# Performance work log

Measured on AMD Instinct MI355X. Metric: run time of the kernel, lower is better.

## Reference

```python
import jax, jax.numpy as jnp
import numpy as np

NUM_HEADS = 16
NUM_FEATURES = 1024
HEAD_DIM = NUM_FEATURES // NUM_HEADS
B, S = 2, 2048


def setup_inputs() -> dict:
    key = jax.random.key(0)
    ks = jax.random.split(key, 12)
    d = NUM_FEATURES
    scale = 1.0 / np.sqrt(d)
    inp = {
        'q': jax.random.normal(ks[0], (B, S, d), jnp.float32),
        'v': jax.random.normal(ks[1], (B, S, d), jnp.float32),
        'k': jax.random.normal(ks[2], (B, S, d), jnp.float32),
        'mask': jnp.ones((1, 1, S, S), jnp.float32),
        # Dense params: flax kernel layout (in, out)
        'Wq': jax.random.normal(ks[3], (d, d), jnp.float32) * scale,
        'bq': jnp.zeros((d,), jnp.float32),
        'Wv': jax.random.normal(ks[4], (d, d), jnp.float32) * scale,
        'bv': jnp.zeros((d,), jnp.float32),
        'Wk': jax.random.normal(ks[5], (d, d), jnp.float32) * scale,
        'bk': jnp.zeros((d,), jnp.float32),
        'Wo': jax.random.normal(ks[6], (d, d), jnp.float32) * scale,
        'bo': jnp.zeros((d,), jnp.float32),
    }
    return inp


def _split_heads(x):
    b, s, _ = x.shape
    return jnp.transpose(x.reshape(b, s, NUM_HEADS, HEAD_DIM), (0, 2, 1, 3))  # [B,H,S,Dh]


def reference(q, v, k, mask, Wq, bq, Wv, bv, Wk, bk, Wo, bo):
    q = q @ Wq + bq
    v = v @ Wv + bv
    k = k @ Wk + bk
    qh = _split_heads(q) / jnp.sqrt(jnp.float32(NUM_FEATURES))  # note: sqrt(d_model), as in source
    kh = _split_heads(k)
    vh = _split_heads(v)
    logits = jnp.einsum('bhqd,bhkd->bhqk', qh, kh)
    logits = logits - 1e9 * (1.0 - mask)
    weights = jax.nn.softmax(logits, axis=-1)
    # dropout deterministic (eval_mode=True) -> identity
    out = jnp.einsum('bhqk,bhkd->bhqd', weights, vh)
    out = jnp.transpose(out, (0, 2, 1, 3)).reshape(q.shape[0], q.shape[1], NUM_FEATURES)
    return out @ Wo + bo
```

## Files before the change

### kernel.cpp

```cpp
#include <hip/hip_runtime.h>
#include <hip/hip_bf16.h>


namespace {
constexpr int DM = 1024;
constexpr int NH = 16;
constexpr int HD = 64;
constexpr int SQ = 2048;
constexpr int M_TOT = 2 * SQ;

using f32x4  = __attribute__((ext_vector_type(4))) float;
using f32x16 = __attribute__((ext_vector_type(16))) float;
using bf16x8 = __attribute__((ext_vector_type(8))) short;
using u16 = unsigned short;

__device__ __forceinline__ u16 f2bf(float f) {
  union { float f; unsigned u; } x; x.f = f;
  unsigned r = x.u + 0x7fffu + ((x.u >> 16) & 1u);
  return (u16)(r >> 16);
}

__device__ __forceinline__ unsigned pk2(float lo, float hi) {
  unsigned r;
  asm("v_cvt_pk_bf16_f32 %0, %1, %2" : "=v"(r) : "v"(lo), "v"(hi));
  return r;
}

__device__ __forceinline__ float fexp2(float x) {
  float r;
  asm("v_exp_f32 %0, %1" : "=v"(r) : "v"(x));
  return r;
}

__device__ __forceinline__ float m3(float a, float b, float c) {
  float r;
  asm("v_max3_f32 %0, %1, %2, %3" : "=v"(r) : "v"(a), "v"(b), "v"(c));
  return r;
}

__device__ __forceinline__ f32x16 mfma32(bf16x8 a, bf16x8 b, f32x16 c) {
  return __builtin_amdgcn_mfma_f32_32x32x16_bf16(a, b, c, 0, 0, 0);
}

__device__ __forceinline__ void gld16(const void* g, void* l) {
  __builtin_amdgcn_global_load_lds((const __attribute__((address_space(1))) void*)g,
                                   (__attribute__((address_space(3))) void*)l, 16, 0, 0);
}
}

__global__ __launch_bounds__(256) void tobf_kernel(const float* __restrict__ q,
                                                   const float* __restrict__ k,
                                                   const float* __restrict__ v,
                                                   u16* __restrict__ out) {
  const float* src = blockIdx.y == 0 ? q : (blockIdx.y == 1 ? k : v);
  u16* dst = out + (size_t)blockIdx.y * M_TOT * DM;
  size_t i = ((size_t)blockIdx.x * 256 + threadIdx.x) * 8;
  float4 a = *(const float4*)(src + i), b = *(const float4*)(src + i + 4);
  union { u16 us[8]; uint4 v4; } pk;
  pk.us[0] = f2bf(a.x); pk.us[1] = f2bf(a.y); pk.us[2] = f2bf(a.z); pk.us[3] = f2bf(a.w);
  pk.us[4] = f2bf(b.x); pk.us[5] = f2bf(b.y); pk.us[6] = f2bf(b.z); pk.us[7] = f2bf(b.w);
  *(uint4*)(dst + i) = pk.v4;
}

__global__ __launch_bounds__(256) void wtrans4_kernel(const float* __restrict__ Wq,
                                                      const float* __restrict__ Wk,
                                                      const float* __restrict__ Wv,
                                                      const float* __restrict__ Wo,
                                                      u16* __restrict__ W3t,
                                                      u16* __restrict__ Wot) {
  const int z = blockIdx.z;
  const float* W = z == 0 ? Wq : (z == 1 ? Wk : (z == 2 ? Wv : Wo));
  u16* Wt = z < 3 ? W3t + (size_t)z * DM * DM : Wot;
  __shared__ u16 tile[64][65];
  const int t = threadIdx.x;
  const int k0 = blockIdx.y * 64, n0 = blockIdx.x * 64;
#pragma unroll
  for (int i = 0; i < 16; ++i) {
    int flat = t + i * 256;
    int kk = flat >> 6, nn = flat & 63;
    tile[kk][nn] = f2bf(W[(size_t)(k0 + kk) * DM + n0 + nn]);
  }
  __syncthreads();
#pragma unroll
  for (int i = 0; i < 16; ++i) {
    int flat = t + i * 256;
    int nn = flat >> 6, kk = flat & 63;
    Wt[(size_t)(n0 + nn) * DM + k0 + kk] = tile[kk][nn];
  }
}

template <int EPI>
__device__ __forceinline__ void gemm_core(const u16* __restrict__ A,
                                          const u16* __restrict__ Wt,
                                          const float* __restrict__ bias,
                                          void* __restrict__ C, float scale,
                                          int m0, int n0, u16* ldsA, u16* ldsB) {
  const int t = threadIdx.x;
  const int lane = t & 63, w = t >> 6;
  const int wm = w >> 1, wn = w & 1;
  const int c = lane & 15, g = lane >> 4;
  const int lr = lane >> 3, lc = lane & 7;
  f32x4 acc[2][4] = {};

  for (int k0 = 0; k0 < DM; k0 += 64) {
    __syncthreads();
#pragma unroll
    for (int j = 0; j < 2; ++j) {
      int row = w * 16 + j * 8 + lr;
      int gc = lc ^ (row & 7);
      gld16(&A[(size_t)(m0 + row) * DM + k0 + gc * 8], (char*)ldsA + w * 2048 + j * 1024);
    }
#pragma unroll
    for (int j = 0; j < 4; ++j) {
      int row = w * 32 + j * 8 + lr;
      int gc = lc ^ (row & 7);
      gld16(&Wt[(size_t)(n0 + row) * DM + k0 + gc * 8], (char*)ldsB + w * 4096 + j * 1024);
    }
    __syncthreads();
#pragma unroll
    for (int ks = 0; ks < 2; ++ks) {
      bf16x8 af[2], bfr[4];
#pragma unroll
      for (int mi = 0; mi < 2; ++mi) {
        int R = wm * 32 + mi * 16 + c;
        af[mi] = *(const bf16x8*)((const char*)ldsA + R * 128 + ((4 * ks + g) ^ (R & 7)) * 16);
      }
#pragma unroll
      for (int ni = 0; ni < 4; ++ni) {
        int R = wn * 64 + ni * 16 + c;
        bfr[ni] = *(const bf16x8*)((const char*)ldsB + R * 128 + ((4 * ks + g) ^ (R & 7)) * 16);
      }
#pragma unroll
      for (int mi = 0; mi < 2; ++mi)
#pragma unroll
        for (int ni = 0; ni < 4; ++ni)
          acc[mi][ni] =
              __builtin_amdgcn_mfma_f32_16x16x32_bf16(af[mi], bfr[ni], acc[mi][ni], 0, 0, 0);
    }
  }
  float bv_[4];
#pragma unroll
  for (int ni = 0; ni < 4; ++ni) bv_[ni] = bias[n0 + wn * 64 + ni * 16 + c];
#pragma unroll
  for (int mi = 0; mi < 2; ++mi) {
#pragma unroll
    for (int ni = 0; ni < 4; ++ni) {
      if (EPI == 1) {
        int mbase = m0 + wm * 32 + mi * 16 + g * 4;
        int n = n0 + wn * 64 + ni * 16 + c;
        int b = mbase >> 11, s = mbase & (SQ - 1);
        int sp = (s & ~12) | ((s & 4) << 1) | ((s & 8) >> 1);
        int h = n >> 6, dh = n & (HD - 1);
        uint2 pkd;
        pkd.x = pk2(acc[mi][ni][0] + bv_[ni], acc[mi][ni][1] + bv_[ni]);
        pkd.y = pk2(acc[mi][ni][2] + bv_[ni], acc[mi][ni][3] + bv_[ni]);
        *(uint2*)&((u16*)C)[((size_t)(b * NH + h) * HD + dh) * SQ + sp] = pkd;
      } else {
#pragma unroll
        for (int r = 0; r < 4; ++r) {
          int m = m0 + wm * 32 + mi * 16 + g * 4 + r;
          int n = n0 + wn * 64 + ni * 16 + c;
          float val = acc[mi][ni][r] + bv_[ni];
          if (EPI == 2) {
            ((float*)C)[(size_t)m * DM + n] = val;
          } else {
            int b = m >> 11, s = m & (SQ - 1);
            int h = n >> 6, dh = n & (HD - 1);
            ((u16*)C)[((size_t)(b * NH + h) * SQ + s) * HD + dh] = f2bf(val * scale);
          }
        }
      }
    }
  }
}

__global__ __launch_bounds__(256) void qkvgemm_kernel(const u16* __restrict__ QKVbf,
                                                      const u16* __restrict__ W3t,
                                                      const float* __restrict__ bq,
                                                      const float* __restrict__ bk,
                                                      const float* __restrict__ bv,
                                                      u16* __restrict__ Qh,
                                                      u16* __restrict__ Kh,
                                                      u16* __restrict__ Vt) {
  __shared__ __align__(16) u16 ldsA[64 * 64];
  __shared__ __align__(16) u16 ldsB[128 * 64];
  int bid = blockIdx.x;
  int swz = (bid & 7) * 192 + (bid >> 3);
  int which = swz >> 9;
  int sub = swz & 511;
  int mt = sub >> 3, nt = sub & 7;
  const u16* A = QKVbf + (size_t)which * M_TOT * DM;
  const u16* Wt = W3t + (size_t)which * DM * DM;
  if (which == 0) {
    gemm_core<0>(A, Wt, bq, Qh, 0.045084222f, mt * 64, nt * 128, ldsA, ldsB);
  } else if (which == 1) {
    gemm_core<0>(A, Wt, bk, Kh, 1.0f, mt * 64, nt * 128, ldsA, ldsB);
  } else {
    gemm_core<1>(A, Wt, bv, Vt, 1.0f, mt * 64, nt * 128, ldsA, ldsB);
  }
}

__global__ __launch_bounds__(256) void ogemm_kernel(const u16* __restrict__ Ob,
                                                    const u16* __restrict__ Wot,
                                                    const float* __restrict__ bo,
                                                    float* __restrict__ out) {
  __shared__ __align__(16) u16 ldsA[64 * 64];
  __shared__ __align__(16) u16 ldsB[128 * 64];
  int bid = blockIdx.x;
  int swz = (bid & 7) * 64 + (bid >> 3);
  int mt = swz >> 3, nt = swz & 7;
  gemm_core<2>(Ob, Wot, bo, out, 1.0f, mt * 64, nt * 128, ldsA, ldsB);
}

__global__ __launch_bounds__(512, 4) void fattn_kernel(const u16* __restrict__ Qh,
                                                       const u16* __restrict__ Kh,
                                                       const u16* __restrict__ Vt,
                                                       u16* __restrict__ Ob) {
  __shared__ __align__(16) u16 ldsKV[2][2][2][64 * 64];
  __shared__ float ldsML[2][8][32];
  const int t = threadIdx.x;
  const int lane = t & 63, w = t >> 6;
  const int l31 = lane & 31, hi = lane >> 5;
  const int wq = w >> 1, wk = w & 1;

  const int bid = blockIdx.x;
  const int swz = (bid & 7) * 64 + (bid >> 3);
  const int bh = swz >> 4, qb = swz & 15;
  const int q0 = qb * 128 + wq * 32;
  const u16* Qb = Qh + (size_t)bh * SQ * HD;
  const u16* Kb = Kh + (size_t)bh * SQ * HD;
  const u16* Vb = Vt + (size_t)bh * HD * SQ;
  const int keybase = wk * (SQ / 2);

  bf16x8 qf[4];
#pragma unroll
  for (int ks = 0; ks < 4; ++ks)
    qf[ks] = *(const bf16x8*)&Qb[(size_t)(q0 + l31) * HD + ks * 16 + hi * 8];

  const short ob = (short)0x3F80;
  const bf16x8 onesv = {ob, ob, ob, ob, ob, ob, ob, ob};

  f32x16 o0 = {}, o1 = {};
  f32x16 lacc = {};
  float m_run = -3e38f;

  auto stage = [&](int kt, int buf) {
#pragma unroll
    for (int j = 0; j < 2; ++j) {
      int r = j * 32 + wq * 8 + (lane >> 3);
      int cg = (lane & 7) ^ (r & 7);
      gld16(&Kb[(size_t)(keybase + kt * 64 + r) * HD + cg * 8],
            (char*)&ldsKV[wk][buf][0][0] + j * 4096 + wq * 1024);
      gld16(&Vb[(size_t)r * SQ + keybase + kt * 64 + cg * 8],
            (char*)&ldsKV[wk][buf][1][0] + j * 4096 + wq * 1024);
    }
  };

  stage(0, 0);
  __syncthreads();

  for (int kt = 0; kt < 16; ++kt) {
    const int cur = kt & 1;
    if (kt + 1 < 16) stage(kt + 1, cur ^ 1);

    f32x16 s0 = {}, s1 = {};
    const char* kbp = (const char*)&ldsKV[wk][cur][0][0];
#pragma unroll
    for (int ks = 0; ks < 4; ++ks) {
      int ch = ((ks * 2 + hi) ^ (l31 & 7)) * 16;
      bf16x8 k0 = *(const bf16x8*)(kbp + l31 * 128 + ch);
      bf16x8 k1 = *(const bf16x8*)(kbp + (32 + l31) * 128 + ch);
      s0 = mfma32(k0, qf[ks], s0);
      s1 = mfma32(k1, qf[ks], s1);
    }

    float t0 = m3(s0[0], s0[1], s0[2]),    t1 = m3(s0[3], s0[4], s0[5]);
    float t2 = m3(s0[6], s0[7], s0[8]),    t3 = m3(s0[9], s0[10], s0[11]);
    float t4 = m3(s0[12], s0[13], s0[14]), t5 = m3(s0[15], s1[0], s1[1]);
    float t6 = m3(s1[2], s1[3], s1[4]),    t7 = m3(s1[5], s1[6], s1[7]);
    float t8 = m3(s1[8], s1[9], s1[10]),   t9 = m3(s1[11], s1[12], s1[13]);
    float t10 = fmaxf(s1[14], s1[15]);
    float u0 = m3(t0, t1, t2), u1 = m3(t3, t4, t5), u2 = m3(t6, t7, t8);
    float u3 = fmaxf(t9, t10);
    float lm = fmaxf(m3(u0, u1, u2), u3);
    float pmax = fmaxf(lm, __shfl_xor(lm, 32));

    if (__any(pmax > m_run + 8.0f)) {
      float mnew = fmaxf(m_run, pmax);
      float scf = fexp2(m_run - mnew);
      m_run = mnew;
#pragma unroll
      for (int r = 0; r < 16; ++r) {
        float sv = __shfl(scf, (r & 3) + 8 * (r >> 2) + 4 * hi);
        o0[r] *= sv;
        o1[r] *= sv;
        lacc[r] *= sv;
      }
    }
#pragma unroll
    for (int r = 0; r < 16; ++r) {
      s0[r] = fexp2(s0[r] - m_run);
      s1[r] = fexp2(s1[r] - m_run);
    }

    union W8 { unsigned u[4]; bf16x8 v; };
    W8 pa[4];
#pragma unroll
    for (int wd = 0; wd < 4; ++wd) {
      pa[0].u[wd] = pk2(s0[2 * wd], s0[2 * wd + 1]);
      pa[1].u[wd] = pk2(s0[8 + 2 * wd], s0[9 + 2 * wd]);
      pa[2].u[wd] = pk2(s1[2 * wd], s1[2 * wd + 1]);
      pa[3].u[wd] = pk2(s1[8 + 2 * wd], s1[9 + 2 * wd]);
    }

    lacc = mfma32(pa[0].v, onesv, lacc);
    lacc = mfma32(pa[1].v, onesv, lacc);
    lacc = mfma32(pa[2].v, onesv, lacc);
    lacc = mfma32(pa[3].v, onesv, lacc);

    const char* vbp = (const char*)&ldsKV[wk][cur][1][0];
#pragma unroll
    for (int g = 0; g < 4; ++g) {
      int ch = ((g * 2 + hi) ^ (l31 & 7)) * 16;
      bf16x8 v0 = *(const bf16x8*)(vbp + l31 * 128 + ch);
      bf16x8 v1 = *(const bf16x8*)(vbp + (32 + l31) * 128 + ch);
      o0 = mfma32(pa[g].v, v0, o0);
      o1 = mfma32(pa[g].v, v1, o1);
    }

    __syncthreads();
  }

  float (*ldsO)[32][64] = (float(*)[32][64]) & ldsKV[0][0][0][0];
#pragma unroll
  for (int r = 0; r < 16; ++r) {
    int q = (r & 3) + 8 * (r >> 2) + 4 * hi;
    ldsO[w][q][l31] = o0[r];
    ldsO[w][q][32 + l31] = o1[r];
  }
  if (hi == 0) ldsML[0][w][l31] = m_run;
  if (l31 == 0) {
#pragma unroll
    for (int r = 0; r < 16; ++r)
      ldsML[1][w][(r & 3) + 8 * (r >> 2) + 4 * hi] = lacc[r];
  }
  __syncthreads();

  {
    const int q = t >> 2;
    const int dh0 = (t & 3) * 16;
    const int wA = (q >> 5) * 2;
    const int ql = q & 31;
    float m0 = ldsML[0][wA][ql], m1 = ldsML[0][wA + 1][ql];
    float l0 = ldsML[1][wA][ql], l1 = ldsML[1][wA + 1][ql];
    float mxv = fmaxf(m0, m1);
    float f0 = fexp2(m0 - mxv), f1 = fexp2(m1 - mxv);
    float inv = 1.0f / (l0 * f0 + l1 * f1);
    union { u16 us[16]; uint4 v4[2]; } pk;
#pragma unroll
    for (int j = 0; j < 16; ++j)
      pk.us[j] = f2bf((ldsO[wA][ql][dh0 + j] * f0 + ldsO[wA + 1][ql][dh0 + j] * f1) * inv);
    const int b = bh >> 4, h = bh & (NH - 1);
    size_t base = ((size_t)b * SQ + qb * 128 + q) * DM + h * HD + dh0;
    *(uint4*)&Ob[base] = pk.v4[0];
    *(uint4*)&Ob[base + 8] = pk.v4[1];
  }
}

extern "C" void kernel_launch(void* const* d_in, const int* in_sizes, int n_in,
                              void* d_out, int out_size, void* d_ws, size_t ws_size,
                              hipStream_t stream) {
  (void)in_sizes; (void)n_in; (void)out_size; (void)ws_size;
  const float* q  = (const float*)d_in[0];
  const float* v  = (const float*)d_in[1];
  const float* k  = (const float*)d_in[2];
  const float* Wq = (const float*)d_in[4];
  const float* bq = (const float*)d_in[5];
  const float* Wv = (const float*)d_in[6];
  const float* bv = (const float*)d_in[7];
  const float* Wk = (const float*)d_in[8];
  const float* bk = (const float*)d_in[9];
  const float* Wo = (const float*)d_in[10];
  const float* bo = (const float*)d_in[11];

  char* ws = (char*)d_ws;
  const size_t MB = 1024 * 1024;
  u16* W3t   = (u16*)(ws + 0 * MB);
  u16* Wot   = (u16*)(ws + 6 * MB);
  u16* QKVbf = (u16*)(ws + 8 * MB);
  u16* Vt    = (u16*)(ws + 32 * MB);
  u16* Ob    = (u16*)(ws + 16 * MB);
  u16* Qh    = (u16*)d_out;
  u16* Kh    = (u16*)d_out + (size_t)4 * 1024 * 1024;

  const dim3 blk(256);
  tobf_kernel<<<dim3(2048, 3), blk, 0, stream>>>(q, k, v, QKVbf);

  wtrans4_kernel<<<dim3(16, 16, 4), blk, 0, stream>>>(Wq, Wk, Wv, Wo, W3t, Wot);

  qkvgemm_kernel<<<dim3(1536), blk, 0, stream>>>(QKVbf, W3t, bq, bk, bv, Qh, Kh, Vt);

  fattn_kernel<<<dim3(512), dim3(512), 0, stream>>>(Qh, Kh, Vt, Ob);

  ogemm_kernel<<<dim3(512), blk, 0, stream>>>(Ob, Wot, bo, (float*)d_out);
}
```

Baseline: 129.2 us.

## Stage V-transpose epilogue through LDS and compute softmax row sums with VALU

The GEMM epilogue that writes the transposed V layout now stages the packed bf16 tile in LDS and then writes 16-byte coalesced rows to global memory, replacing the scattered 8-byte strided stores. Separately, the attention kernel drops the MFMA-with-ones trick for accumulating softmax denominators and instead sums the exponentials per lane in registers, combining lane halves with one shuffle at the end. The first aims to cut uncoalesced write traffic and the second to remove four MFMAs per key tile. The costs are two extra barriers plus LDS reuse in the epilogue, and additional VALU adds in the attention loop.

Result: faster. 115.8 us (-10.4%).

```diff
diff --git a/kernel.cpp b/kernel.cpp
--- a/kernel.cpp
+++ b/kernel.cpp
@@ -141,37 +141,54 @@
   float bv_[4];
 #pragma unroll
   for (int ni = 0; ni < 4; ++ni) bv_[ni] = bias[n0 + wn * 64 + ni * 16 + c];
-#pragma unroll
-  for (int mi = 0; mi < 2; ++mi) {
-#pragma unroll
-    for (int ni = 0; ni < 4; ++ni) {
-      if (EPI == 1) {
-        int mbase = m0 + wm * 32 + mi * 16 + g * 4;
-        int n = n0 + wn * 64 + ni * 16 + c;
-        int b = mbase >> 11, s = mbase & (SQ - 1);
-        int sp = (s & ~12) | ((s & 4) << 1) | ((s & 8) >> 1);
-        int h = n >> 6, dh = n & (HD - 1);
+
+  if (EPI == 1) {
+    __syncthreads();
+#pragma unroll
+    for (int mi = 0; mi < 2; ++mi) {
+#pragma unroll
+      for (int ni = 0; ni < 4; ++ni) {
+        int n_local = wn * 64 + ni * 16 + c;
+        int mb = wm * 32 + mi * 16 + g * 4;
+        int mp = (mb & ~12) | ((mb & 4) << 1) | ((mb & 8) >> 1);
         uint2 pkd;
         pkd.x = pk2(acc[mi][ni][0] + bv_[ni], acc[mi][ni][1] + bv_[ni]);
         pkd.y = pk2(acc[mi][ni][2] + bv_[ni], acc[mi][ni][3] + bv_[ni]);
-        *(uint2*)&((u16*)C)[((size_t)(b * NH + h) * HD + dh) * SQ + sp] = pkd;
-      } else {
-#pragma unroll
-        for (int r = 0; r < 4; ++r) {
-          int m = m0 + wm * 32 + mi * 16 + g * 4 + r;
-          int n = n0 + wn * 64 + ni * 16 + c;
-          float val = acc[mi][ni][r] + bv_[ni];
-          if (EPI == 2) {
-            ((float*)C)[(size_t)m * DM + n] = val;
-          } else {
-            int b = m >> 11, s = m & (SQ - 1);
-            int h = n >> 6, dh = n & (HD - 1);
-            ((u16*)C)[((size_t)(b * NH + h) * SQ + s) * HD + dh] = f2bf(val * scale);
-          }
+        int chunk = (mp >> 3) ^ (n_local & 7);
+        *(uint2*)((char*)ldsB + n_local * 128 + chunk * 16 + (mp & 7) * 2) = pkd;
+      }
+    }
+    __syncthreads();
+    const int b = m0 >> 11, s0g = m0 & (SQ - 1);
+#pragma unroll
+    for (int p = 0; p < 4; ++p) {
+      int n_local = p * 32 + (t >> 3);
+      int ch = t & 7;
+      uint4 v = *(const uint4*)((const char*)ldsB + n_local * 128 + ((ch ^ (n_local & 7)) * 16));
+      int n_g = n0 + n_local;
+      int h = n_g >> 6, dh = n_g & (HD - 1);
+      *(uint4*)&((u16*)C)[((size_t)(b * NH + h) * HD + dh) * SQ + s0g + ch * 8] = v;
+    }
+    return;
+  }
+
+#pragma unroll
+  for (int mi = 0; mi < 2; ++mi)
+#pragma unroll
+    for (int ni = 0; ni < 4; ++ni)
+#pragma unroll
+      for (int r = 0; r < 4; ++r) {
+        int m = m0 + wm * 32 + mi * 16 + g * 4 + r;
+        int n = n0 + wn * 64 + ni * 16 + c;
+        float val = acc[mi][ni][r] + bv_[ni];
+        if (EPI == 2) {
+          ((float*)C)[(size_t)m * DM + n] = val;
+        } else {
+          int b = m >> 11, s = m & (SQ - 1);
+          int h = n >> 6, dh = n & (HD - 1);
+          ((u16*)C)[((size_t)(b * NH + h) * SQ + s) * HD + dh] = f2bf(val * scale);
         }
       }
-    }
-  }
 }
 
 __global__ __launch_bounds__(256) void qkvgemm_kernel(const u16* __restrict__ QKVbf,
@@ -237,12 +254,8 @@
   for (int ks = 0; ks < 4; ++ks)
     qf[ks] = *(const bf16x8*)&Qb[(size_t)(q0 + l31) * HD + ks * 16 + hi * 8];
 
-  const short ob = (short)0x3F80;
-  const bf16x8 onesv = {ob, ob, ob, ob, ob, ob, ob, ob};
-
   f32x16 o0 = {}, o1 = {};
-  f32x16 lacc = {};
-  float m_run = -3e38f;
+  float m_run = -3e38f, l_run = 0.f;
 
   auto stage = [&](int kt, int buf) {
 #pragma unroll
@@ -289,12 +302,12 @@
       float mnew = fmaxf(m_run, pmax);
       float scf = fexp2(m_run - mnew);
       m_run = mnew;
+      l_run *= scf;
 #pragma unroll
       for (int r = 0; r < 16; ++r) {
         float sv = __shfl(scf, (r & 3) + 8 * (r >> 2) + 4 * hi);
         o0[r] *= sv;
         o1[r] *= sv;
-        lacc[r] *= sv;
       }
     }
 #pragma unroll
@@ -302,6 +315,14 @@
       s0[r] = fexp2(s0[r] - m_run);
       s1[r] = fexp2(s1[r] - m_run);
     }
+    float sm[16];
+#pragma unroll
+    for (int r = 0; r < 16; ++r) sm[r] = s0[r] + s1[r];
+#pragma unroll
+    for (int d = 8; d >= 1; d >>= 1)
+#pragma unroll
+      for (int r = 0; r < d; ++r) sm[r] += sm[r + d];
+    l_run += sm[0];
 
     union W8 { unsigned u[4]; bf16x8 v; };
     W8 pa[4];
@@ -312,11 +333,6 @@
       pa[2].u[wd] = pk2(s1[2 * wd], s1[2 * wd + 1]);
       pa[3].u[wd] = pk2(s1[8 + 2 * wd], s1[9 + 2 * wd]);
     }
-
-    lacc = mfma32(pa[0].v, onesv, lacc);
-    lacc = mfma32(pa[1].v, onesv, lacc);
-    lacc = mfma32(pa[2].v, onesv, lacc);
-    lacc = mfma32(pa[3].v, onesv, lacc);
 
     const char* vbp = (const char*)&ldsKV[wk][cur][1][0];
 #pragma unroll
@@ -331,6 +347,7 @@
     __syncthreads();
   }
 
+  float l2 = l_run + __shfl_xor(l_run, 32);
   float (*ldsO)[32][64] = (float(*)[32][64]) & ldsKV[0][0][0][0];
 #pragma unroll
   for (int r = 0; r < 16; ++r) {
@@ -338,11 +355,9 @@
     ldsO[w][q][l31] = o0[r];
     ldsO[w][q][32 + l31] = o1[r];
   }
-  if (hi == 0) ldsML[0][w][l31] = m_run;
-  if (l31 == 0) {
-#pragma unroll
-    for (int r = 0; r < 16; ++r)
-      ldsML[1][w][(r & 3) + 8 * (r >> 2) + 4 * hi] = lacc[r];
+  if (hi == 0) {
+    ldsML[0][w][l31] = m_run;
+    ldsML[1][w][l31] = l2;
   }
   __syncthreads();
 
```
